# Kernel optimization log

Measured on AMD Instinct MI355X. Metric: run time of the kernel, lower is better.

## Reference

```python
import jax, jax.numpy as jnp
import numpy as np

B, S, D = 16, 4096, 1024
DIM_K, DIM_V, NUM_HEAD = 1024, 1024, 16


def setup_inputs() -> dict:
    key = jax.random.key(0)
    ks = jax.random.split(key, 7)
    s_in = 1.0 / np.sqrt(D)
    return {
        "x": jax.random.normal(ks[0], (B, S, D), dtype=jnp.float32),
        "Wq": jax.random.normal(ks[1], (D, DIM_K), dtype=jnp.float32) * s_in,
        "bq": jnp.zeros((DIM_K,), dtype=jnp.float32),
        "Wk": jax.random.normal(ks[2], (D, DIM_K), dtype=jnp.float32) * s_in,
        "bk": jnp.zeros((DIM_K,), dtype=jnp.float32),
        "Wv": jax.random.normal(ks[3], (D, DIM_V), dtype=jnp.float32) * s_in,
        "bv": jnp.zeros((DIM_V,), dtype=jnp.float32),
    }


def reference(x, Wq, bq, Wk, bk, Wv, bv):
    H = NUM_HEAD
    b, s, _ = x.shape
    Q = x @ Wq + bq                      # (B,S,dim_k)
    K = x @ Wk + bk                      # (B,S,dim_k)
    V = x @ Wv + bv                      # (B,S,dim_v)
    Q_ = Q.reshape(b, s, H, DIM_K // H)  # (B,S,H,dk)
    K_ = K.reshape(b, s, H, DIM_K // H)
    V_ = V.reshape(b, s, H, DIM_V // H)
    # NOTE: faithful to the source quirk — scores are across HEADS (H x H)
    # at each (batch, seq) position; no 1/sqrt(dim_k) scaling (unused in source).
    scores = jnp.einsum("bshd,bsgd->bshg", Q_, K_)   # (B,S,H,H)
    atten = jax.nn.softmax(scores, axis=-1)
    out = jnp.einsum("bshg,bsgd->bshd", atten, V_)    # (B,S,H,dv_head)
    return out.reshape(b, s, -1)                      # (B,S,dim_v)
```

## Files before the change

kernel.cpp:

```cpp
#include <hip/hip_runtime.h>
#include <stdint.h>

#define M_TOTAL 65536
#define DIM     1024
#define NQKV    3072
#define NHEAD   16
#define HDIM    64

typedef __attribute__((ext_vector_type(8))) _Float16 f16x8;
typedef __attribute__((ext_vector_type(4))) _Float16 f16x4;
typedef __attribute__((ext_vector_type(4))) float    f32x4;

__global__ __launch_bounds__(256) void cvt_x_kernel(const float* __restrict__ x,
                                                    _Float16* __restrict__ xh,
                                                    int n4) {
    int i = blockIdx.x * blockDim.x + threadIdx.x;
    int stride = gridDim.x * blockDim.x;
    const float4* x4 = (const float4*)x;
    f16x4* o4 = (f16x4*)xh;
    for (; i < n4; i += stride) {
        float4 v = x4[i];
        f16x4 o;
        o[0] = (_Float16)v.x; o[1] = (_Float16)v.y;
        o[2] = (_Float16)v.z; o[3] = (_Float16)v.w;
        o4[i] = o;
    }
}

__global__ void cvt_w_kernel(const float* __restrict__ Wq,
                             const float* __restrict__ Wk,
                             const float* __restrict__ Wv,
                             _Float16* __restrict__ Wt) {
    __shared__ float tile[32][33];
    int which = blockIdx.z;
    const float* W = (which == 0) ? Wq : (which == 1) ? Wk : Wv;
    int d0 = blockIdx.y * 32, n0 = blockIdx.x * 32;
    int tx = threadIdx.x, ty = threadIdx.y;
    tile[ty][tx] = W[(size_t)(d0 + ty) * DIM + n0 + tx];
    __syncthreads();
    Wt[(size_t)(which * DIM + n0 + ty) * DIM + d0 + tx] = (_Float16)tile[tx][ty];
}

__global__ __launch_bounds__(256) void bias_kernel(const float* __restrict__ bq,
                                                   const float* __restrict__ bk,
                                                   const float* __restrict__ bv,
                                                   float* __restrict__ bias) {
    int i = blockIdx.x * 256 + threadIdx.x;
    if (i < NQKV)
        bias[i] = (i < 1024) ? bq[i] : (i < 2048) ? bk[i - 1024] : bv[i - 2048];
}


#define LDSA(slot)  ((slot) << 15)
#define LDSB(slot)  (65536 + ((slot) << 15))

#define MFMA16(AF, BF, MB, NB)                                                  \
    __builtin_amdgcn_s_setprio(1);                                              \
    _Pragma("unroll") for (int mi = 0; mi < 4; ++mi)                            \
    _Pragma("unroll") for (int ni = 0; ni < 2; ++ni)                            \
    _Pragma("unroll") for (int ks = 0; ks < 2; ++ks)                            \
        acc[(MB) + mi][(NB) + ni] = __builtin_amdgcn_mfma_f32_16x16x32_f16(     \
            BF[ni][ks], AF[mi][ks], acc[(MB) + mi][(NB) + ni], 0, 0, 0);        \
    __builtin_amdgcn_s_setprio(0);

#define LGKM(n)  do { asm volatile("s_waitcnt lgkmcnt(" #n ")" ::: "memory");   \
                      __builtin_amdgcn_sched_barrier(0); } while (0)
#define VMCNT(n) do { asm volatile("s_waitcnt vmcnt(" #n ")" ::: "memory");     \
                      __builtin_amdgcn_sched_barrier(0); } while (0)

__global__ __launch_bounds__(512, 2) void qkv_gemm_kernel(const _Float16* __restrict__ Xh,
                                                          const _Float16* __restrict__ Wth,
                                                          const float* __restrict__ bias,
                                                          _Float16* __restrict__ Ch) {
    extern __shared__ char smem[];

    const int bid = blockIdx.x;
    const int swz = (bid & 7) * (3072 / 8) + (bid >> 3);
    const int tm  = swz / (NQKV / 256);
    const int tn  = swz % (NQKV / 256);
    const int brow = tm * 256;
    const int bcol = tn * 256;

    const int tid = threadIdx.x;
    const int w   = tid >> 6;
    const int l   = tid & 63;
    const int wm  = w >> 2;
    const int wn  = w & 3;

    const int lrow8 = l >> 3;
    const int lcol8 = (l & 7) ^ lrow8;
    const _Float16* pAsrc = Xh  + (size_t)(brow + w * 8 + lrow8) * DIM + lcol8 * 8;
    const _Float16* pBsrc = Wth + (size_t)(bcol + w * 8 + lrow8) * DIM + lcol8 * 8;

    auto stageA = [&](int slot, int kt) {
#pragma unroll
        for (int ln = 0; ln < 4; ++ln) {
            const _Float16* s = pAsrc + (size_t)(ln * 64) * DIM + ((size_t)kt << 6);
            char* d = smem + LDSA(slot) + ln * 8192 + (w << 10);
            __builtin_amdgcn_global_load_lds((const __attribute__((address_space(1))) void*)s,
                                             (__attribute__((address_space(3))) void*)d, 16, 0, 0);
        }
    };
    auto stageB = [&](int slot, int kt) {
#pragma unroll
        for (int ln = 0; ln < 4; ++ln) {
            const _Float16* s = pBsrc + (size_t)(ln * 64) * DIM + ((size_t)kt << 6);
            char* d = smem + LDSB(slot) + ln * 8192 + (w << 10);
            __builtin_amdgcn_global_load_lds((const __attribute__((address_space(1))) void*)s,
                                             (__attribute__((address_space(3))) void*)d, 16, 0, 0);
        }
    };

    const int aRowB = ((wm << 7) + (l & 15)) << 7;
    const int bRowB = 65536 + (((wn << 6) + (l & 15)) << 7);
    const int xk0 = (((l >> 4) ^ (l & 7)) << 4);
    const int xk1 = ((((l >> 4) + 4) ^ (l & 7)) << 4);
    auto LDA = [&](int slot, int mi, int ks) -> f16x8 {
        return *(const f16x8*)(smem + (slot << 15) + aRowB + (mi << 11) + (ks ? xk1 : xk0));
    };
    auto LDB = [&](int slot, int ni, int ks) -> f16x8 {
        return *(const f16x8*)(smem + (slot << 15) + bRowB + (ni << 11) + (ks ? xk1 : xk0));
    };

    f32x4 acc[8][4] = {};
    f16x8 aA[4][2], aB[4][2], bA[2][2], bB[2][2];

    auto READ_A0 = [&](int slot) {
#pragma unroll
        for (int mi = 0; mi < 4; ++mi) { aA[mi][0] = LDA(slot, mi, 0); aA[mi][1] = LDA(slot, mi, 1); }
    };
    auto READ_A4 = [&](int slot) {
#pragma unroll
        for (int mi = 0; mi < 4; ++mi) { aB[mi][0] = LDA(slot, mi + 4, 0); aB[mi][1] = LDA(slot, mi + 4, 1); }
    };
    auto READ_B0 = [&](int slot) {
#pragma unroll
        for (int ni = 0; ni < 2; ++ni) { bA[ni][0] = LDB(slot, ni, 0); bA[ni][1] = LDB(slot, ni, 1); }
    };
    auto READ_B2 = [&](int slot) {
#pragma unroll
        for (int ni = 0; ni < 2; ++ni) { bB[ni][0] = LDB(slot, ni + 2, 0); bB[ni][1] = LDB(slot, ni + 2, 1); }
    };

    stageA(0, 0); stageB(0, 0);
    stageA(1, 1); stageB(1, 1);
    VMCNT(8);
    __builtin_amdgcn_s_barrier();
    READ_A0(0); READ_B0(0);

#pragma unroll 1
    for (int u = 0; u < 14; ++u) {
        const int s = u & 1;
        READ_B2(s);  LGKM(4);  MFMA16(aA, bA, 0, 0)
        READ_A4(s);  LGKM(8);  MFMA16(aA, bB, 0, 2)
        READ_B0(s);  LGKM(4);  MFMA16(aB, bB, 4, 2)
        LGKM(0);
        __builtin_amdgcn_s_barrier();
        stageA(s, u + 2); stageB(s, u + 2);
        MFMA16(aB, bA, 4, 0)
        VMCNT(8);
        __builtin_amdgcn_s_barrier();
        READ_A0(1 - s); READ_B0(1 - s);
    }

    READ_B2(0);  LGKM(4);  MFMA16(aA, bA, 0, 0)
    READ_A4(0);  LGKM(8);  MFMA16(aA, bB, 0, 2)
    READ_B0(0);  LGKM(4);  MFMA16(aB, bB, 4, 2)
    LGKM(0);
    MFMA16(aB, bA, 4, 0)
    VMCNT(0);
    __builtin_amdgcn_s_barrier();
    READ_A0(1); READ_B0(1);

    READ_B2(1);  LGKM(4);  MFMA16(aA, bA, 0, 0)
    READ_A4(1);  LGKM(8);  MFMA16(aA, bB, 0, 2)
    READ_B0(1);  LGKM(4);  MFMA16(aB, bB, 4, 2)
    LGKM(0);
    MFMA16(aB, bA, 4, 0)

    __syncthreads();
#pragma unroll
    for (int mi = 0; mi < 8; ++mi) {
        const int m = (wm << 7) + (mi << 4) + (l & 15);
        const int msw = m & 7;
#pragma unroll
        for (int ni = 0; ni < 4; ++ni) {
            const int n0 = (wn << 6) + (ni << 4) + ((l >> 4) << 2);
            const float4 bv4 = *(const float4*)&bias[bcol + n0];
            f16x4 h;
            h[0] = (_Float16)(acc[mi][ni][0] + bv4.x);
            h[1] = (_Float16)(acc[mi][ni][1] + bv4.y);
            h[2] = (_Float16)(acc[mi][ni][2] + bv4.z);
            h[3] = (_Float16)(acc[mi][ni][3] + bv4.w);
            const int c8 = n0 >> 2;
            *(f16x4*)(smem + m * 512 + (((c8 >> 1) ^ msw) << 4) + ((c8 & 1) << 3)) = h;
        }
    }
    __syncthreads();
#pragma unroll
    for (int it = 0; it < 16; ++it) {
        const int row = (tid >> 5) + (it << 4);
        const int c16 = tid & 31;
        f16x8 vv = *(const f16x8*)(smem + row * 512 + ((c16 ^ (row & 7)) << 4));
        *(f16x8*)&Ch[(size_t)(brow + row) * NQKV + bcol + (c16 << 3)] = vv;
    }
}

__global__ __launch_bounds__(256) void attn_kernel(const _Float16* __restrict__ QKVh,
                                                   float* __restrict__ out) {
    __shared__ _Float16 vlds[4][1024];
    __shared__ float attlds[4][16][16];

    const int w = threadIdx.x >> 6, l = threadIdx.x & 63;
    const size_t p = (size_t)blockIdx.x * 4 + w;
    const _Float16* base = QKVh + p * NQKV;
    const _Float16* qrow = base;
    const _Float16* krow = base + 1024;
    const _Float16* vrow = base + 2048;
    const int h = l & 15;
    const int g4 = (l >> 4) * 4;

    *(uint4*)&vlds[w][l * 16]     = *(const uint4*)&vrow[l * 16];
    *(uint4*)&vlds[w][l * 16 + 8] = *(const uint4*)&vrow[l * 16 + 8];

    const int fo = (l & 15) * HDIM + (l >> 4) * 8;
    f16x8 aK0 = *(const f16x8*)&krow[fo];
    f16x8 aK1 = *(const f16x8*)&krow[fo + 32];
    f16x8 bQ0 = *(const f16x8*)&qrow[fo];
    f16x8 bQ1 = *(const f16x8*)&qrow[fo + 32];

    f32x4 sT = {0.f, 0.f, 0.f, 0.f};
    sT = __builtin_amdgcn_mfma_f32_16x16x32_f16(aK0, bQ0, sT, 0, 0, 0);
    sT = __builtin_amdgcn_mfma_f32_16x16x32_f16(aK1, bQ1, sT, 0, 0, 0);

    float m = fmaxf(fmaxf(sT[0], sT[1]), fmaxf(sT[2], sT[3]));
    m = fmaxf(m, __shfl_xor(m, 16));
    m = fmaxf(m, __shfl_xor(m, 32));
    float e0 = __expf(sT[0] - m), e1 = __expf(sT[1] - m);
    float e2 = __expf(sT[2] - m), e3 = __expf(sT[3] - m);
    float s = e0 + e1 + e2 + e3;
    s += __shfl_xor(s, 16);
    s += __shfl_xor(s, 32);
    const float inv = 1.0f / s;

    float4 att = make_float4(e0 * inv, e1 * inv, e2 * inv, e3 * inv);
    *(float4*)&attlds[w][h][g4] = att;
    __syncthreads();

    const int dbase = (l >> 4) * 16;
    float acc[16];
#pragma unroll
    for (int c = 0; c < 16; ++c) acc[c] = 0.f;

#pragma unroll
    for (int g = 0; g < 16; ++g) {
        const float av = attlds[w][h][g];
        f16x8 v0 = *(const f16x8*)&vlds[w][g * HDIM + dbase];
        f16x8 v1 = *(const f16x8*)&vlds[w][g * HDIM + dbase + 8];
#pragma unroll
        for (int c = 0; c < 8; ++c) {
            acc[c]     += av * (float)v0[c];
            acc[c + 8] += av * (float)v1[c];
        }
    }

    float* op = out + p * DIM + h * HDIM + dbase;
#pragma unroll
    for (int c = 0; c < 16; c += 4)
        *(float4*)(op + c) = make_float4(acc[c], acc[c + 1], acc[c + 2], acc[c + 3]);
}

extern "C" void kernel_launch(void* const* d_in, const int* in_sizes, int n_in,
                              void* d_out, int out_size, void* d_ws, size_t ws_size,
                              hipStream_t stream) {
    const float* x  = (const float*)d_in[0];
    const float* Wq = (const float*)d_in[1];
    const float* bq = (const float*)d_in[2];
    const float* Wk = (const float*)d_in[3];
    const float* bk = (const float*)d_in[4];
    const float* Wv = (const float*)d_in[5];
    const float* bv = (const float*)d_in[6];
    float* out = (float*)d_out;

    char* ws = (char*)d_ws;
    _Float16* Xh  = (_Float16*)ws;
    _Float16* Wth = (_Float16*)(ws + 134217728);
    float*    bias = (float*)(ws + 134217728 + 6291456);
    _Float16* Ch  = (_Float16*)(ws + 134217728 + 6291456 + 12288);

    (void)hipFuncSetAttribute((const void*)qkv_gemm_kernel,
                              hipFuncAttributeMaxDynamicSharedMemorySize, 131072);

    hipLaunchKernelGGL(cvt_x_kernel, dim3(2048), dim3(256), 0, stream,
                       x, Xh, (M_TOTAL * DIM) / 4);
    hipLaunchKernelGGL(cvt_w_kernel, dim3(32, 32, 3), dim3(32, 32), 0, stream,
                       Wq, Wk, Wv, Wth);
    hipLaunchKernelGGL(bias_kernel, dim3(12), dim3(256), 0, stream,
                       bq, bk, bv, bias);
    hipLaunchKernelGGL(qkv_gemm_kernel, dim3((M_TOTAL / 256) * (NQKV / 256)), dim3(512), 131072, stream,
                       Xh, Wth, bias, Ch);
    hipLaunchKernelGGL(attn_kernel, dim3(M_TOTAL / 4), dim3(256), 0, stream,
                       Ch, out);
}
```

Before: 646.7 us.

## Restructure GEMM main loop into ping-pong schedule with extra barriers

```diff
diff --git a/kernel.cpp b/kernel.cpp
--- a/kernel.cpp
+++ b/kernel.cpp
@@ -54,7 +54,7 @@
 #define LDSA(slot)  ((slot) << 15)
 #define LDSB(slot)  (65536 + ((slot) << 15))
 
-#define MFMA16(AF, BF, MB, NB)                                                  \
+#define MFMAQ(AF, BF, MB, NB)                                                   \
     __builtin_amdgcn_s_setprio(1);                                              \
     _Pragma("unroll") for (int mi = 0; mi < 4; ++mi)                            \
     _Pragma("unroll") for (int ni = 0; ni < 2; ++ni)                            \
@@ -63,10 +63,39 @@
             BF[ni][ks], AF[mi][ks], acc[(MB) + mi][(NB) + ni], 0, 0, 0);        \
     __builtin_amdgcn_s_setprio(0);
 
-#define LGKM(n)  do { asm volatile("s_waitcnt lgkmcnt(" #n ")" ::: "memory");   \
-                      __builtin_amdgcn_sched_barrier(0); } while (0)
-#define VMCNT(n) do { asm volatile("s_waitcnt vmcnt(" #n ")" ::: "memory");     \
-                      __builtin_amdgcn_sched_barrier(0); } while (0)
+#define SB0      __builtin_amdgcn_sched_barrier(0)
+#define BARRIER  __builtin_amdgcn_s_barrier()
+#define LGKM0    do { asm volatile("s_waitcnt lgkmcnt(0)" ::: "memory"); SB0; } while (0)
+#define VMW(n)   do { asm volatile("s_waitcnt vmcnt(" #n ")" ::: "memory"); SB0; } while (0)
+
+#define TILE_FULL(S, KT, VMN)                                                   \
+    READ_BB(S); READ_AB(S); SB0;                                                \
+    MFMAQ(aA, bA, 0, 0)                                                         \
+    BARRIER;                                                                    \
+    MFMAQ(aA, bB, 0, 2)                                                         \
+    LGKM0;                                                                      \
+    BARRIER;                                                                    \
+    stageA((S), (KT)); stageB((S), (KT));                                       \
+    MFMAQ(aB, bA, 4, 0)                                                         \
+    VMW(VMN);                                                                   \
+    BARRIER;                                                                    \
+    READ_AA(1 - (S)); READ_BA(1 - (S)); SB0;                                    \
+    MFMAQ(aB, bB, 4, 2)                                                         \
+    BARRIER;
+
+#define TILE_NOSTAGE(S, VMN)                                                    \
+    READ_BB(S); READ_AB(S); SB0;                                                \
+    MFMAQ(aA, bA, 0, 0)                                                         \
+    BARRIER;                                                                    \
+    MFMAQ(aA, bB, 0, 2)                                                         \
+    LGKM0;                                                                      \
+    BARRIER;                                                                    \
+    MFMAQ(aB, bA, 4, 0)                                                         \
+    VMW(VMN);                                                                   \
+    BARRIER;                                                                    \
+    READ_AA(1 - (S)); READ_BA(1 - (S)); SB0;                                    \
+    MFMAQ(aB, bB, 4, 2)                                                         \
+    BARRIER;
 
 __global__ __launch_bounds__(512, 2) void qkv_gemm_kernel(const _Float16* __restrict__ Xh,
                                                           const _Float16* __restrict__ Wth,
@@ -125,58 +154,44 @@
     f32x4 acc[8][4] = {};
     f16x8 aA[4][2], aB[4][2], bA[2][2], bB[2][2];
 
-    auto READ_A0 = [&](int slot) {
+    auto READ_AA = [&](int slot) {
 #pragma unroll
         for (int mi = 0; mi < 4; ++mi) { aA[mi][0] = LDA(slot, mi, 0); aA[mi][1] = LDA(slot, mi, 1); }
     };
-    auto READ_A4 = [&](int slot) {
+    auto READ_AB = [&](int slot) {
 #pragma unroll
         for (int mi = 0; mi < 4; ++mi) { aB[mi][0] = LDA(slot, mi + 4, 0); aB[mi][1] = LDA(slot, mi + 4, 1); }
     };
-    auto READ_B0 = [&](int slot) {
+    auto READ_BA = [&](int slot) {
 #pragma unroll
         for (int ni = 0; ni < 2; ++ni) { bA[ni][0] = LDB(slot, ni, 0); bA[ni][1] = LDB(slot, ni, 1); }
     };
-    auto READ_B2 = [&](int slot) {
+    auto READ_BB = [&](int slot) {
 #pragma unroll
         for (int ni = 0; ni < 2; ++ni) { bB[ni][0] = LDB(slot, ni + 2, 0); bB[ni][1] = LDB(slot, ni + 2, 1); }
     };
 
     stageA(0, 0); stageB(0, 0);
     stageA(1, 1); stageB(1, 1);
-    VMCNT(8);
-    __builtin_amdgcn_s_barrier();
-    READ_A0(0); READ_B0(0);
+    VMW(8);
+    BARRIER;
+    SB0;
+    READ_AA(0); READ_BA(0);
 
 #pragma unroll 1
-    for (int u = 0; u < 14; ++u) {
-        const int s = u & 1;
-        READ_B2(s);  LGKM(4);  MFMA16(aA, bA, 0, 0)
-        READ_A4(s);  LGKM(8);  MFMA16(aA, bB, 0, 2)
-        READ_B0(s);  LGKM(4);  MFMA16(aB, bB, 4, 2)
-        LGKM(0);
-        __builtin_amdgcn_s_barrier();
-        stageA(s, u + 2); stageB(s, u + 2);
-        MFMA16(aB, bA, 4, 0)
-        VMCNT(8);
-        __builtin_amdgcn_s_barrier();
-        READ_A0(1 - s); READ_B0(1 - s);
-    }
-
-    READ_B2(0);  LGKM(4);  MFMA16(aA, bA, 0, 0)
-    READ_A4(0);  LGKM(8);  MFMA16(aA, bB, 0, 2)
-    READ_B0(0);  LGKM(4);  MFMA16(aB, bB, 4, 2)
-    LGKM(0);
-    MFMA16(aB, bA, 4, 0)
-    VMCNT(0);
-    __builtin_amdgcn_s_barrier();
-    READ_A0(1); READ_B0(1);
-
-    READ_B2(1);  LGKM(4);  MFMA16(aA, bA, 0, 0)
-    READ_A4(1);  LGKM(8);  MFMA16(aA, bB, 0, 2)
-    READ_B0(1);  LGKM(4);  MFMA16(aB, bB, 4, 2)
-    LGKM(0);
-    MFMA16(aB, bA, 4, 0)
+    for (int i = 0; i < 7; ++i) {
+        const int u = 2 * i;
+        TILE_FULL(0, u + 2, 8)
+        TILE_FULL(1, u + 3, 8)
+    }
+
+    TILE_NOSTAGE(0, 0)
+
+    READ_BB(1); READ_AB(1); SB0;
+    MFMAQ(aA, bA, 0, 0)
+    MFMAQ(aA, bB, 0, 2)
+    MFMAQ(aB, bA, 4, 0)
+    MFMAQ(aB, bB, 4, 2)
 
     __syncthreads();
 #pragma unroll
```

Measured after the change: 645.3 us. About the same (-0.2%).
